# Kernel optimization log

Hardware: AMD Instinct MI355X
Metric: run time of the kernel (lower is better)

Reference implementation:

```python
import jax, jax.numpy as jnp
import numpy as np

B, N_MM, N_V, N_A = 2, 256, 64, 128
DIM, HEADS, ATTN_RATIO, MLP_RATIO = 1024, 16, 0.25, 4.0
INNER = int(DIM * ATTN_RATIO)          # 256
HID = int(DIM * MLP_RATIO)             # 4096
SCALE = (DIM // HEADS) ** -0.5         # faithful to source: uses dim//num_heads
EPS = 1e-5


def setup_inputs() -> dict:
    key = jax.random.key(0)
    ks = jax.random.split(key, 16)
    s = 0.02
    return {
        "xmm": jax.random.normal(ks[0], (B, N_MM, DIM), jnp.float32),
        "xv": jax.random.normal(ks[1], (B, N_V, DIM), jnp.float32),
        "xa": jax.random.normal(ks[2], (B, N_A, DIM), jnp.float32),
        "ln_mm_w": jnp.ones((DIM,), jnp.float32),
        "ln_mm_b": jnp.zeros((DIM,), jnp.float32),
        "ln_v_w": jnp.ones((DIM,), jnp.float32),
        "ln_v_b": jnp.zeros((DIM,), jnp.float32),
        "ln_a_w": jnp.ones((DIM,), jnp.float32),
        "ln_a_b": jnp.zeros((DIM,), jnp.float32),
        "Wq": jax.random.normal(ks[3], (DIM, INNER), jnp.float32) * s,
        "Wkv": jax.random.normal(ks[4], (2 * DIM, 2 * INNER), jnp.float32) * s,
        "Wproj": jax.random.normal(ks[5], (INNER, DIM), jnp.float32) * s,
        "bproj": jnp.zeros((DIM,), jnp.float32),
        "ln_mlp_w": jnp.ones((DIM,), jnp.float32),
        "ln_mlp_b": jnp.zeros((DIM,), jnp.float32),
        "W1": jax.random.normal(ks[6], (DIM, HID), jnp.float32) * s,
        "b1": jnp.zeros((HID,), jnp.float32),
        "W2": jax.random.normal(ks[7], (HID, DIM), jnp.float32) * s,
        "b2": jnp.zeros((DIM,), jnp.float32),
    }


def _ln(x, w, b):
    m = x.mean(-1, keepdims=True)
    v = ((x - m) ** 2).mean(-1, keepdims=True)
    return (x - m) / jnp.sqrt(v + EPS) * w + b


def reference(xmm, xv, xa, ln_mm_w, ln_mm_b, ln_v_w, ln_v_b, ln_a_w, ln_a_b,
              Wq, Wkv, Wproj, bproj, ln_mlp_w, ln_mlp_b, W1, b1, W2, b2):
    hd = INNER // HEADS
    src_mm = _ln(xmm, ln_mm_w, ln_mm_b)
    src_v = _ln(xv, ln_v_w, ln_v_b)
    src_a = _ln(xa, ln_a_w, ln_a_b)

    # kv(x_va) where x_va = cat([xv broadcast over N_a, xa broadcast over N_v], -1).
    # Equivalent to projecting each stream separately and broadcast-adding:
    kv_v = src_v @ Wkv[:DIM]            # [B, N_v, 2*INNER]
    kv_a = src_a @ Wkv[DIM:]            # [B, N_a, 2*INNER]
    kv = kv_v[:, :, None, :] + kv_a[:, None, :, :]          # [B, N_v, N_a, 2*INNER]
    kv = kv.reshape(B, N_V * N_A, 2, HEADS, hd)
    k = kv[:, :, 0].transpose(0, 2, 1, 3)                   # [B, H, N_va, hd]
    v = kv[:, :, 1].transpose(0, 2, 1, 3)

    q = (src_mm @ Wq).reshape(B, N_MM, HEADS, hd).transpose(0, 2, 1, 3)

    attn = jnp.einsum('bhqd,bhkd->bhqk', q, k) * SCALE
    attn = jax.nn.softmax(attn, axis=-1)
    out = jnp.einsum('bhqk,bhkd->bhqd', attn, v)
    out = out.transpose(0, 2, 1, 3).reshape(B, N_MM, INNER)
    out = out @ Wproj + bproj

    xmm = xmm + out
    h = _ln(xmm, ln_mlp_w, ln_mlp_b)
    h = jax.nn.gelu(h @ W1 + b1, approximate=False) @ W2 + b2
    return xmm + h
```

## Files before the change

### kernel.cpp

```cpp
#include <hip/hip_runtime.h>
#include <hip/hip_bf16.h>
#include <math.h>


typedef unsigned short ushort_t;
typedef __attribute__((ext_vector_type(8))) __bf16 bf16x8;
typedef __attribute__((ext_vector_type(4))) float f32x4;

#define DEVFN static __device__ __forceinline__

DEVFN ushort_t f2bf(float f) {
    unsigned int x = __float_as_uint(f);
    unsigned int r = x + 0x7FFFu + ((x >> 16) & 1u);
    return (ushort_t)(r >> 16);
}
DEVFN void unpack8(uint4 dv, float* dst) {
    unsigned int ws[4] = {dv.x, dv.y, dv.z, dv.w};
#pragma unroll
    for (int i = 0; i < 4; i++) {
        dst[2 * i] = __uint_as_float(ws[i] << 16);
        dst[2 * i + 1] = __uint_as_float(ws[i] & 0xFFFF0000u);
    }
}

DEVFN void ln_body(const float* __restrict__ x, const float* __restrict__ w,
                   const float* __restrict__ b, ushort_t* __restrict__ out,
                   int row) {
    const float4* xr4 = (const float4*)(x + (size_t)row * 1024);
    ushort_t* orow = out + (size_t)row * 1024;
    int tid = threadIdx.x;
    float4 v4 = xr4[tid];
    float s = v4.x + v4.y + v4.z + v4.w;
    float ss = v4.x * v4.x + v4.y * v4.y + v4.z * v4.z + v4.w * v4.w;
#pragma unroll
    for (int off = 32; off > 0; off >>= 1) {
        s += __shfl_down(s, off);
        ss += __shfl_down(ss, off);
    }
    __shared__ float red[8];
    if ((tid & 63) == 0) {
        red[tid >> 6] = s;
        red[4 + (tid >> 6)] = ss;
    }
    __syncthreads();
    s = red[0] + red[1] + red[2] + red[3];
    ss = red[4] + red[5] + red[6] + red[7];
    float mean = s * (1.f / 1024.f);
    float var = ss * (1.f / 1024.f) - mean * mean;
    float rstd = rsqrtf(var + 1e-5f);
    const float4 w4 = ((const float4*)w)[tid];
    const float4 b4 = ((const float4*)b)[tid];
    union { ushort_t u[4]; uint2 v; } pk;
    pk.u[0] = f2bf((v4.x - mean) * rstd * w4.x + b4.x);
    pk.u[1] = f2bf((v4.y - mean) * rstd * w4.y + b4.y);
    pk.u[2] = f2bf((v4.z - mean) * rstd * w4.z + b4.z);
    pk.u[3] = f2bf((v4.w - mean) * rstd * w4.w + b4.w);
    *(uint2*)(&orow[tid * 4]) = pk.v;
}

__global__ __launch_bounds__(256) void ln_kernel(
    const float* __restrict__ x, const float* __restrict__ w,
    const float* __restrict__ b, ushort_t* __restrict__ out) {
    ln_body(x, w, b, out, blockIdx.x);
}

struct LNSeg {
    const float* x; const float* w; const float* b; ushort_t* out; int start;
};
struct TDesc { const float* in; ushort_t* out; int R, C, nx, start; };

DEVFN void transpose_body(TDesc d, int t, ushort_t* lds) {
    int bx = (t % d.nx) * 64;
    int by = (t / d.nx) * 64;
    int tid = threadIdx.x;
#pragma unroll
    for (int it = 0; it < 4; it++) {
        int idx = it * 256 + tid;
        int r = idx >> 4;
        int c4 = (idx & 15) << 2;
        float4 v = *(const float4*)(&d.in[(size_t)(by + r) * d.C + bx + c4]);
        float vals[4] = {v.x, v.y, v.z, v.w};
#pragma unroll
        for (int j = 0; j < 4; j++) {
            int c = c4 + j;
            int rs = (r + (((c >> 2) & 7) << 3)) & 63;
            lds[c * 64 + rs] = f2bf(vals[j]);
        }
    }
    __syncthreads();
#pragma unroll
    for (int it = 0; it < 2; it++) {
        int idx = it * 256 + tid;
        int c = idx >> 3;
        int l8 = idx & 7;
        int rs = ((l8 << 3) + (((c >> 2) & 7) << 3)) & 63;
        uint4 val = *(const uint4*)(&lds[c * 64 + rs]);
        *(uint4*)(&d.out[(size_t)(bx + c) * d.R + by + (l8 << 3)]) = val;
    }
    __syncthreads();
}

__global__ __launch_bounds__(256) void prep_kernel(LNSeg l0, LNSeg l1,
                                                   LNSeg l2, TDesc d0,
                                                   TDesc d1) {
    int id = blockIdx.x;
    if (id < 896) {
        LNSeg s = (id >= l2.start) ? l2 : ((id >= l1.start) ? l1 : l0);
        ln_body(s.x, s.w, s.b, s.out, id - s.start);
        return;
    }
    id -= 896;
    __shared__ ushort_t tile[64 * 64];
    TDesc d = (id >= d1.start) ? d1 : d0;
    transpose_body(d, id - d.start, tile);
}

template <int EPI, typename OutT>
DEVFN void gemm64_core(const ushort_t* __restrict__ A, int lda,
                       const ushort_t* __restrict__ B, int ldb,
                       OutT* __restrict__ C, int ldc,
                       const float* __restrict__ bias,
                       const float* __restrict__ resid, int K, int m0, int n0,
                       ushort_t* As, ushort_t* Bs) {
    constexpr int LS = 72;
    int tid = threadIdx.x;
    int wave = tid >> 6, lane = tid & 63;
    int wm = wave >> 1, wn = wave & 1;
    int quad = lane >> 4, l16 = lane & 15;

    f32x4 acc[2][2];
#pragma unroll
    for (int i = 0; i < 2; i++)
#pragma unroll
        for (int j = 0; j < 2; j++) acc[i][j] = (f32x4){0.f, 0.f, 0.f, 0.f};

    int r = tid >> 3;
    int c = tid & 7;
    const ushort_t* Ap = A + (size_t)(m0 + r) * lda + c * 8;
    const ushort_t* Bp = B + (size_t)(n0 + r) * ldb + c * 8;
    const ushort_t* Ap2 = Ap + (size_t)32 * lda;
    const ushort_t* Bp2 = Bp + (size_t)32 * ldb;
    uint4 ra = *(const uint4*)Ap, ra2 = *(const uint4*)Ap2;
    uint4 rb = *(const uint4*)Bp, rb2 = *(const uint4*)Bp2;

    for (int k0 = 0; k0 < K; k0 += 64) {
        *(uint4*)(&As[r * LS + c * 8]) = ra;
        *(uint4*)(&As[(r + 32) * LS + c * 8]) = ra2;
        *(uint4*)(&Bs[r * LS + c * 8]) = rb;
        *(uint4*)(&Bs[(r + 32) * LS + c * 8]) = rb2;
        __syncthreads();
        if (k0 + 64 < K) {
            ra = *(const uint4*)(Ap + k0 + 64);
            ra2 = *(const uint4*)(Ap2 + k0 + 64);
            rb = *(const uint4*)(Bp + k0 + 64);
            rb2 = *(const uint4*)(Bp2 + k0 + 64);
        }
#pragma unroll
        for (int ks = 0; ks < 2; ks++) {
            bf16x8 af[2], bfr[2];
#pragma unroll
            for (int i = 0; i < 2; i++)
                af[i] = *(const bf16x8*)(
                    &As[(wm * 32 + i * 16 + l16) * LS + ks * 32 + quad * 8]);
#pragma unroll
            for (int j = 0; j < 2; j++)
                bfr[j] = *(const bf16x8*)(
                    &Bs[(wn * 32 + j * 16 + l16) * LS + ks * 32 + quad * 8]);
#pragma unroll
            for (int i = 0; i < 2; i++)
#pragma unroll
                for (int j = 0; j < 2; j++)
                    acc[i][j] = __builtin_amdgcn_mfma_f32_16x16x32_bf16(
                        af[i], bfr[j], acc[i][j], 0, 0, 0);
        }
        __syncthreads();
    }

#pragma unroll
    for (int i = 0; i < 2; i++)
#pragma unroll
        for (int j = 0; j < 2; j++) {
            int col = n0 + wn * 32 + j * 16 + l16;
            int rbase = m0 + wm * 32 + i * 16 + quad * 4;
            float bv = (EPI == 2 || EPI == 3) ? bias[col] : 0.f;
#pragma unroll
            for (int rr = 0; rr < 4; rr++) {
                int row = rbase + rr;
                float vv = acc[i][j][rr] + bv;
                if (EPI == 2) vv = 0.5f * vv * (1.f + erff(vv * 0.70710678118654752f));
                if (EPI == 3) vv += resid[(size_t)row * ldc + col];
                if constexpr (sizeof(OutT) == 2)
                    C[(size_t)row * ldc + col] = (OutT)f2bf(vv);
                else
                    C[(size_t)row * ldc + col] = vv;
            }
        }
}

template <int EPI, typename OutT>
__global__ __launch_bounds__(256) void gemm64(
    const ushort_t* __restrict__ A, int lda, const ushort_t* __restrict__ Bt,
    int ldb, OutT* __restrict__ C, int ldc, const float* __restrict__ bias,
    const float* __restrict__ resid, int Kper, int sliceStride) {
    __shared__ ushort_t As[64 * 72];
    __shared__ ushort_t Bs[64 * 72];
    int z = blockIdx.z;
    gemm64_core<EPI, OutT>(A + (size_t)z * Kper, lda, Bt + (size_t)z * Kper,
                           ldb, C + (size_t)z * sliceStride, ldc, bias, resid,
                           Kper, blockIdx.y * 64, blockIdx.x * 64, As, Bs);
}

struct GSeg {
    const ushort_t* A; const ushort_t* B; ushort_t* C;
    int lda, ldb, ldc, nx, start;
};

__global__ __launch_bounds__(256) void projT_kernel(GSeg s0, GSeg s1, GSeg s2,
                                                    TDesc d0, TDesc d1,
                                                    TDesc d2, int K) {
    __shared__ ushort_t As[64 * 72];
    __shared__ ushort_t Bs[64 * 72];
    int id = blockIdx.x;
    if (id < 80) {
        GSeg s = (id >= s2.start) ? s2 : ((id >= s1.start) ? s1 : s0);
        int t = id - s.start;
        int n0 = (t % s.nx) * 64;
        int m0 = (t / s.nx) * 64;
        gemm64_core<0, ushort_t>(s.A, s.lda, s.B, s.ldb, s.C, s.ldc, nullptr,
                                 nullptr, K, m0, n0, As, Bs);
        return;
    }
    id -= 80;
    TDesc d = (id >= d2.start) ? d2 : ((id >= d1.start) ? d1 : d0);
    transpose_body(d, id - d.start, As);
}

__global__ __launch_bounds__(256) void reduce_mlp2(
    const float* __restrict__ P, const float* __restrict__ y,
    const float* __restrict__ b2, float* __restrict__ out) {
    int i = blockIdx.x * 256 + threadIdx.x;
    const float4* p = (const float4*)P;
    float4 a = p[i], b = p[i + 131072], cc = p[i + 2 * 131072],
           d = p[i + 3 * 131072];
    float4 yy = ((const float4*)y)[i];
    float4 bb = ((const float4*)b2)[i & 255];
    float4 o;
    o.x = a.x + b.x + cc.x + d.x + yy.x + bb.x;
    o.y = a.y + b.y + cc.y + d.y + yy.y + bb.y;
    o.z = a.z + b.z + cc.z + d.z + yy.z + bb.z;
    o.w = a.w + b.w + cc.w + d.w + yy.w + bb.w;
    ((float4*)out)[i] = o;
}

__global__ __launch_bounds__(256) void attn_kernel(
    const ushort_t* __restrict__ q, const ushort_t* __restrict__ kvv,
    const ushort_t* __restrict__ kva, ushort_t* __restrict__ out) {
    int bh = blockIdx.x;
    int b = bh >> 4, h = bh & 15;
    int tid = threadIdx.x;

    __shared__ float Kv[64][16], Vv[64][16], Ka[128][16], Va[128][16];

    {
        int row = tid >> 2, seg = (tid >> 1) & 1, half = tid & 1;
        const ushort_t* src =
            kvv + (size_t)(b * 64 + row) * 512 + seg * 256 + h * 16 + half * 8;
        float* dst = (seg ? Vv[row] : Kv[row]) + half * 8;
        unpack8(*(const uint4*)src, dst);
    }
#pragma unroll
    for (int t2 = 0; t2 < 2; t2++) {
        int t = tid + t2 * 256;
        int row = t >> 2, seg = (t >> 1) & 1, half = t & 1;
        const ushort_t* src =
            kva + (size_t)(b * 128 + row) * 512 + seg * 256 + h * 16 + half * 8;
        float* dst = (seg ? Va[row] : Ka[row]) + half * 8;
        unpack8(*(const uint4*)src, dst);
    }
    __syncthreads();

    int qlocal = tid >> 2;
    int dg = tid & 3;
    int qrow = blockIdx.y * 64 + qlocal;
    const ushort_t* qp = q + (size_t)(b * 256 + qrow) * 256 + h * 16 + dg * 4;
    uint2 qu = *(const uint2*)qp;
    float4 qv;
    qv.x = __uint_as_float(qu.x << 16) * 0.125f;
    qv.y = __uint_as_float(qu.x & 0xFFFF0000u) * 0.125f;
    qv.z = __uint_as_float(qu.y << 16) * 0.125f;
    qv.w = __uint_as_float(qu.y & 0xFFFF0000u) * 0.125f;

    const float4* Kv4 = (const float4*)Kv;
    const float4* Vv4 = (const float4*)Vv;
    const float4* Ka4 = (const float4*)Ka;
    const float4* Va4 = (const float4*)Va;

    float4 ov = {0.f, 0.f, 0.f, 0.f};
    float den = 0.f;
#pragma unroll 8
    for (int i = 0; i < 64; i++) {
        float4 kk = Kv4[i * 4 + dg];
        float part = qv.x * kk.x + qv.y * kk.y + qv.z * kk.z + qv.w * kk.w;
        part += __shfl_xor(part, 1);
        part += __shfl_xor(part, 2);
        float p = __expf(part);
        den += p;
        float4 vv = Vv4[i * 4 + dg];
        ov.x += p * vv.x; ov.y += p * vv.y; ov.z += p * vv.z; ov.w += p * vv.w;
    }
    float4 oa = {0.f, 0.f, 0.f, 0.f};
    float dena = 0.f;
#pragma unroll 8
    for (int i = 0; i < 128; i++) {
        float4 kk = Ka4[i * 4 + dg];
        float part = qv.x * kk.x + qv.y * kk.y + qv.z * kk.z + qv.w * kk.w;
        part += __shfl_xor(part, 1);
        part += __shfl_xor(part, 2);
        float p = __expf(part);
        dena += p;
        float4 vv = Va4[i * 4 + dg];
        oa.x += p * vv.x; oa.y += p * vv.y; oa.z += p * vv.z; oa.w += p * vv.w;
    }

    float rv = 1.f / den, ra = 1.f / dena;
    union { ushort_t u[4]; uint2 v; } pk;
    pk.u[0] = f2bf(ov.x * rv + oa.x * ra);
    pk.u[1] = f2bf(ov.y * rv + oa.y * ra);
    pk.u[2] = f2bf(ov.z * rv + oa.z * ra);
    pk.u[3] = f2bf(ov.w * rv + oa.w * ra);
    *(uint2*)(out + (size_t)(b * 256 + qrow) * 256 + h * 16 + dg * 4) = pk.v;
}

extern "C" void kernel_launch(void* const* d_in, const int* in_sizes, int n_in,
                              void* d_out, int out_size, void* d_ws,
                              size_t ws_size, hipStream_t stream) {
    const float* xmm = (const float*)d_in[0];
    const float* xv = (const float*)d_in[1];
    const float* xa = (const float*)d_in[2];
    const float* ln_mm_w = (const float*)d_in[3];
    const float* ln_mm_b = (const float*)d_in[4];
    const float* ln_v_w = (const float*)d_in[5];
    const float* ln_v_b = (const float*)d_in[6];
    const float* ln_a_w = (const float*)d_in[7];
    const float* ln_a_b = (const float*)d_in[8];
    const float* Wq = (const float*)d_in[9];
    const float* Wkv = (const float*)d_in[10];
    const float* Wproj = (const float*)d_in[11];
    const float* bproj = (const float*)d_in[12];
    const float* ln_mlp_w = (const float*)d_in[13];
    const float* ln_mlp_b = (const float*)d_in[14];
    const float* W1 = (const float*)d_in[15];
    const float* b1 = (const float*)d_in[16];
    const float* W2 = (const float*)d_in[17];
    const float* b2 = (const float*)d_in[18];
    float* outp = (float*)d_out;

    char* w = (char*)d_ws;
    ushort_t* xmmN = (ushort_t*)w;    w += 512 * 1024 * 2;
    ushort_t* xvN = (ushort_t*)w;     w += 128 * 1024 * 2;
    ushort_t* xaN = (ushort_t*)w;     w += 256 * 1024 * 2;
    ushort_t* Wqt = (ushort_t*)w;     w += 256 * 1024 * 2;
    ushort_t* Wkvt = (ushort_t*)w;    w += 512 * 2048 * 2;
    ushort_t* Wprojt = (ushort_t*)w;  w += 1024 * 256 * 2;
    ushort_t* W1t = (ushort_t*)w;     w += 4096 * 1024 * 2;
    ushort_t* W2t = (ushort_t*)w;     w += 1024 * 4096 * 2;
    ushort_t* qout = (ushort_t*)w;    w += 512 * 256 * 2;
    ushort_t* kvvb = (ushort_t*)w;    w += 128 * 512 * 2;
    ushort_t* kvab = (ushort_t*)w;    w += 256 * 512 * 2;
    ushort_t* attnout = (ushort_t*)w; w += 512 * 256 * 2;
    float* y = (float*)w;             w += 512 * 1024 * 4;
    ushort_t* h0 = (ushort_t*)w;      w += 512 * 1024 * 2;
    ushort_t* g = (ushort_t*)w;       w += 512 * 4096 * 2;
    float* P = (float*)w;             w += 4 * 512 * 1024 * 4;

    LNSeg L0{xmm, ln_mm_w, ln_mm_b, xmmN, 0};
    LNSeg L1{xv, ln_v_w, ln_v_b, xvN, 512};
    LNSeg L2{xa, ln_a_w, ln_a_b, xaN, 640};
    TDesc TQ{Wq, Wqt, 1024, 256, 4, 0};
    TDesc TKV{Wkv, Wkvt, 2048, 512, 8, 64};
    prep_kernel<<<896 + 320, 256, 0, stream>>>(L0, L1, L2, TQ, TKV);

    GSeg G0{xmmN, Wqt, qout, 1024, 1024, 256, 4, 0};
    GSeg G1{xvN, Wkvt, kvvb, 1024, 2048, 512, 8, 32};
    GSeg G2{xaN, Wkvt + 1024, kvab, 1024, 2048, 512, 8, 48};
    TDesc TP{Wproj, Wprojt, 256, 1024, 16, 0};
    TDesc T1{W1, W1t, 1024, 4096, 64, 64};
    TDesc T2{W2, W2t, 4096, 1024, 16, 1088};
    projT_kernel<<<80 + 2112, 256, 0, stream>>>(G0, G1, G2, TP, T1, T2, 1024);

    attn_kernel<<<dim3(32, 4), 256, 0, stream>>>(qout, kvvb, kvab, attnout);

    gemm64<3, float><<<dim3(16, 8, 1), 256, 0, stream>>>(
        attnout, 256, Wprojt, 256, y, 1024, bproj, xmm, 256, 0);

    ln_kernel<<<512, 256, 0, stream>>>(y, ln_mlp_w, ln_mlp_b, h0);

    gemm64<2, ushort_t><<<dim3(64, 8, 1), 256, 0, stream>>>(
        h0, 1024, W1t, 1024, g, 4096, b1, nullptr, 1024, 0);

    gemm64<4, float><<<dim3(16, 8, 4), 256, 0, stream>>>(
        g, 4096, W2t, 4096, P, 1024, nullptr, nullptr, 1024, 512 * 1024);

    reduce_mlp2<<<512, 256, 0, stream>>>(P, y, b2, outp);

    (void)in_sizes; (void)n_in; (void)out_size; (void)ws_size;
}
```

Before: 184.2 us.

## Fuse attention, projection, LN and MLP stages into one persistent kernel with grid barriers

Six separate tail launches (attention, output projection, MLP LayerNorm, two MLP GEMMs, split-K reduction) are merged into one 512-block kernel. Stages are separated by software grid-wide barriers built on atomic counters in workspace, which are zeroed by a memset each call. The aim is to remove per-launch overhead and the idle gaps between small kernels. The cost is spin-wait barriers: they assume all 512 blocks are resident at once (launch bounds request 2 blocks per CU), and the loop breaks out after a fixed retry count, which could silently break correctness if co-residency fails.

```diff
diff --git a/kernel.cpp b/kernel.cpp
--- a/kernel.cpp
+++ b/kernel.cpp
@@ -21,6 +21,22 @@
         dst[2 * i] = __uint_as_float(ws[i] << 16);
         dst[2 * i + 1] = __uint_as_float(ws[i] & 0xFFFF0000u);
     }
+}
+
+DEVFN void gsync(unsigned int* c) {
+    __syncthreads();
+    if (threadIdx.x == 0) {
+        __threadfence();
+        __hip_atomic_fetch_add(c, 1u, __ATOMIC_RELEASE, __HIP_MEMORY_SCOPE_AGENT);
+        unsigned int nb = gridDim.x;
+        unsigned int tries = 0;
+        while (__hip_atomic_load(c, __ATOMIC_ACQUIRE, __HIP_MEMORY_SCOPE_AGENT) < nb) {
+            __builtin_amdgcn_s_sleep(1);
+            if (++tries > (1u << 22)) break;
+        }
+        __threadfence();
+    }
+    __syncthreads();
 }
 
 DEVFN void ln_body(const float* __restrict__ x, const float* __restrict__ w,
@@ -58,12 +74,6 @@
     *(uint2*)(&orow[tid * 4]) = pk.v;
 }
 
-__global__ __launch_bounds__(256) void ln_kernel(
-    const float* __restrict__ x, const float* __restrict__ w,
-    const float* __restrict__ b, ushort_t* __restrict__ out) {
-    ln_body(x, w, b, out, blockIdx.x);
-}
-
 struct LNSeg {
     const float* x; const float* w; const float* b; ushort_t* out; int start;
 };
@@ -195,19 +205,6 @@
                     C[(size_t)row * ldc + col] = vv;
             }
         }
-}
-
-template <int EPI, typename OutT>
-__global__ __launch_bounds__(256) void gemm64(
-    const ushort_t* __restrict__ A, int lda, const ushort_t* __restrict__ Bt,
-    int ldb, OutT* __restrict__ C, int ldc, const float* __restrict__ bias,
-    const float* __restrict__ resid, int Kper, int sliceStride) {
-    __shared__ ushort_t As[64 * 72];
-    __shared__ ushort_t Bs[64 * 72];
-    int z = blockIdx.z;
-    gemm64_core<EPI, OutT>(A + (size_t)z * Kper, lda, Bt + (size_t)z * Kper,
-                           ldb, C + (size_t)z * sliceStride, ldc, bias, resid,
-                           Kper, blockIdx.y * 64, blockIdx.x * 64, As, Bs);
 }
 
 struct GSeg {
@@ -235,31 +232,16 @@
     transpose_body(d, id - d.start, As);
 }
 
-__global__ __launch_bounds__(256) void reduce_mlp2(
-    const float* __restrict__ P, const float* __restrict__ y,
-    const float* __restrict__ b2, float* __restrict__ out) {
-    int i = blockIdx.x * 256 + threadIdx.x;
-    const float4* p = (const float4*)P;
-    float4 a = p[i], b = p[i + 131072], cc = p[i + 2 * 131072],
-           d = p[i + 3 * 131072];
-    float4 yy = ((const float4*)y)[i];
-    float4 bb = ((const float4*)b2)[i & 255];
-    float4 o;
-    o.x = a.x + b.x + cc.x + d.x + yy.x + bb.x;
-    o.y = a.y + b.y + cc.y + d.y + yy.y + bb.y;
-    o.z = a.z + b.z + cc.z + d.z + yy.z + bb.z;
-    o.w = a.w + b.w + cc.w + d.w + yy.w + bb.w;
-    ((float4*)out)[i] = o;
-}
-
-__global__ __launch_bounds__(256) void attn_kernel(
-    const ushort_t* __restrict__ q, const ushort_t* __restrict__ kvv,
-    const ushort_t* __restrict__ kva, ushort_t* __restrict__ out) {
-    int bh = blockIdx.x;
+DEVFN void attn_body(const ushort_t* __restrict__ q,
+                     const ushort_t* __restrict__ kvv,
+                     const ushort_t* __restrict__ kva,
+                     ushort_t* __restrict__ out, int bh, int qc, float* sm) {
     int b = bh >> 4, h = bh & 15;
     int tid = threadIdx.x;
-
-    __shared__ float Kv[64][16], Vv[64][16], Ka[128][16], Va[128][16];
+    float (*Kv)[16] = (float(*)[16])sm;
+    float (*Vv)[16] = (float(*)[16])(sm + 64 * 16);
+    float (*Ka)[16] = (float(*)[16])(sm + 2 * 64 * 16);
+    float (*Va)[16] = (float(*)[16])(sm + 2 * 64 * 16 + 128 * 16);
 
     {
         int row = tid >> 2, seg = (tid >> 1) & 1, half = tid & 1;
@@ -281,7 +263,7 @@
 
     int qlocal = tid >> 2;
     int dg = tid & 3;
-    int qrow = blockIdx.y * 64 + qlocal;
+    int qrow = qc * 64 + qlocal;
     const ushort_t* qp = q + (size_t)(b * 256 + qrow) * 256 + h * 16 + dg * 4;
     uint2 qu = *(const uint2*)qp;
     float4 qv;
@@ -329,6 +311,74 @@
     pk.u[2] = f2bf(ov.z * rv + oa.z * ra);
     pk.u[3] = f2bf(ov.w * rv + oa.w * ra);
     *(uint2*)(out + (size_t)(b * 256 + qrow) * 256 + h * 16 + dg * 4) = pk.v;
+}
+
+DEVFN void reduce_body(const float* __restrict__ P, const float* __restrict__ y,
+                       const float* __restrict__ b2, float* __restrict__ out,
+                       int blk) {
+    int i = blk * 256 + threadIdx.x;
+    const float4* p = (const float4*)P;
+    float4 a = p[i], b = p[i + 131072], cc = p[i + 2 * 131072],
+           d = p[i + 3 * 131072];
+    float4 yy = ((const float4*)y)[i];
+    float4 bb = ((const float4*)b2)[i & 255];
+    float4 o;
+    o.x = a.x + b.x + cc.x + d.x + yy.x + bb.x;
+    o.y = a.y + b.y + cc.y + d.y + yy.y + bb.y;
+    o.z = a.z + b.z + cc.z + d.z + yy.z + bb.z;
+    o.w = a.w + b.w + cc.w + d.w + yy.w + bb.w;
+    ((float4*)out)[i] = o;
+}
+
+struct TailArgs {
+    const ushort_t* qout; const ushort_t* kvvb; const ushort_t* kvab;
+    ushort_t* attnout;
+    const ushort_t* Wprojt; const float* bproj; const float* xmm; float* y;
+    const float* ln_mlp_w; const float* ln_mlp_b; ushort_t* h0;
+    const ushort_t* W1t; const float* b1; ushort_t* g;
+    const ushort_t* W2t; float* P;
+    const float* b2; float* outp;
+    unsigned int* bars;
+};
+
+__global__ __launch_bounds__(256, 2) void tail_kernel(TailArgs a) {
+    __shared__ __align__(16) char smem[24576];
+    ushort_t* As = (ushort_t*)smem;
+    ushort_t* Bs = (ushort_t*)(smem + 9216);
+    int bid = blockIdx.x;
+
+    if (bid < 128) attn_body(a.qout, a.kvvb, a.kvab, a.attnout, bid & 31,
+                             bid >> 5, (float*)smem);
+    gsync(&a.bars[0]);
+
+    if (bid < 128) {
+        int n0 = (bid % 16) * 64, m0 = (bid / 16) * 64;
+        gemm64_core<3, float>(a.attnout, 256, a.Wprojt, 256, a.y, 1024,
+                              a.bproj, a.xmm, 256, m0, n0, As, Bs);
+    }
+    gsync(&a.bars[1]);
+
+    ln_body(a.y, a.ln_mlp_w, a.ln_mlp_b, a.h0, bid);
+    gsync(&a.bars[2]);
+
+    {
+        int n0 = (bid % 64) * 64, m0 = (bid / 64) * 64;
+        gemm64_core<2, ushort_t>(a.h0, 1024, a.W1t, 1024, a.g, 4096, a.b1,
+                                 nullptr, 1024, m0, n0, As, Bs);
+    }
+    gsync(&a.bars[3]);
+
+    {
+        int z = bid >> 7, rr = bid & 127;
+        int n0 = (rr % 16) * 64, m0 = (rr / 16) * 64;
+        gemm64_core<4, float>(a.g + (size_t)z * 1024, 4096,
+                              a.W2t + (size_t)z * 1024, 4096,
+                              a.P + (size_t)z * 512 * 1024, 1024, nullptr,
+                              nullptr, 1024, m0, n0, As, Bs);
+    }
+    gsync(&a.bars[4]);
+
+    reduce_body(a.P, a.y, a.b2, a.outp, bid);
 }
 
 extern "C" void kernel_launch(void* const* d_in, const int* in_sizes, int n_in,
@@ -356,6 +406,7 @@
     float* outp = (float*)d_out;
 
     char* w = (char*)d_ws;
+    unsigned int* bars = (unsigned int*)w; w += 256;
     ushort_t* xmmN = (ushort_t*)w;    w += 512 * 1024 * 2;
     ushort_t* xvN = (ushort_t*)w;     w += 128 * 1024 * 2;
     ushort_t* xaN = (ushort_t*)w;     w += 256 * 1024 * 2;
@@ -373,6 +424,8 @@
     ushort_t* g = (ushort_t*)w;       w += 512 * 4096 * 2;
     float* P = (float*)w;             w += 4 * 512 * 1024 * 4;
 
+    hipMemsetAsync(bars, 0, 64, stream);
+
     LNSeg L0{xmm, ln_mm_w, ln_mm_b, xmmN, 0};
     LNSeg L1{xv, ln_v_w, ln_v_b, xvN, 512};
     LNSeg L2{xa, ln_a_w, ln_a_b, xaN, 640};
@@ -388,20 +441,13 @@
     TDesc T2{W2, W2t, 4096, 1024, 16, 1088};
     projT_kernel<<<80 + 2112, 256, 0, stream>>>(G0, G1, G2, TP, T1, T2, 1024);
 
-    attn_kernel<<<dim3(32, 4), 256, 0, stream>>>(qout, kvvb, kvab, attnout);
-
-    gemm64<3, float><<<dim3(16, 8, 1), 256, 0, stream>>>(
-        attnout, 256, Wprojt, 256, y, 1024, bproj, xmm, 256, 0);
-
-    ln_kernel<<<512, 256, 0, stream>>>(y, ln_mlp_w, ln_mlp_b, h0);
-
-    gemm64<2, ushort_t><<<dim3(64, 8, 1), 256, 0, stream>>>(
-        h0, 1024, W1t, 1024, g, 4096, b1, nullptr, 1024, 0);
-
-    gemm64<4, float><<<dim3(16, 8, 4), 256, 0, stream>>>(
-        g, 4096, W2t, 4096, P, 1024, nullptr, nullptr, 1024, 512 * 1024);
-
-    reduce_mlp2<<<512, 256, 0, stream>>>(P, y, b2, outp);
+    TailArgs TA{qout, kvvb, kvab, attnout,
+                Wprojt, bproj, xmm, y,
+                ln_mlp_w, ln_mlp_b, h0,
+                W1t, b1, g,
+                W2t, P,
+                b2, outp, bars};
+    tail_kernel<<<512, 256, 0, stream>>>(TA);
 
     (void)in_sizes; (void)n_in; (void)out_size; (void)ws_size;
 }
```

After: 512.4 us. 2.78x slower.

## Fuse MLP LayerNorm into GEMMs and split-K reduction into last block

Applied to the files above, without the earlier changes.

The proj GEMM epilogue now writes per-tile row sum and sum-of-squares partials. The W1 GEMM reads those partials to normalize y on the fly, which removes the separate LayerNorm kernel and the h0 buffer. The split-K reduction for W2 is folded into the GEMM through an atomic counter: the last of the four slices per tile does the sum, which removes another launch. The costs are a variance computed as E[x²]-mean² from partials, an fp32 A-operand load with per-element conversion inside the W1 GEMM loop, and counter resets placed in the attention kernel.

```diff
diff --git a/kernel.cpp b/kernel.cpp
--- a/kernel.cpp
+++ b/kernel.cpp
@@ -58,12 +58,6 @@
     *(uint2*)(&orow[tid * 4]) = pk.v;
 }
 
-__global__ __launch_bounds__(256) void ln_kernel(
-    const float* __restrict__ x, const float* __restrict__ w,
-    const float* __restrict__ b, ushort_t* __restrict__ out) {
-    ln_body(x, w, b, out, blockIdx.x);
-}
-
 struct LNSeg {
     const float* x; const float* w; const float* b; ushort_t* out; int start;
 };
@@ -121,7 +115,8 @@
                        OutT* __restrict__ C, int ldc,
                        const float* __restrict__ bias,
                        const float* __restrict__ resid, int K, int m0, int n0,
-                       ushort_t* As, ushort_t* Bs) {
+                       ushort_t* As, ushort_t* Bs,
+                       float* __restrict__ stats = nullptr) {
     constexpr int LS = 72;
     int tid = threadIdx.x;
     int wave = tid >> 6, lane = tid & 63;
@@ -176,38 +171,58 @@
         __syncthreads();
     }
 
+    float srow[2][4] = {{0.f, 0.f, 0.f, 0.f}, {0.f, 0.f, 0.f, 0.f}};
+    float ssrow[2][4] = {{0.f, 0.f, 0.f, 0.f}, {0.f, 0.f, 0.f, 0.f}};
+
 #pragma unroll
     for (int i = 0; i < 2; i++)
 #pragma unroll
         for (int j = 0; j < 2; j++) {
             int col = n0 + wn * 32 + j * 16 + l16;
             int rbase = m0 + wm * 32 + i * 16 + quad * 4;
-            float bv = (EPI == 2 || EPI == 3) ? bias[col] : 0.f;
+            float bv = (EPI == 5) ? bias[col] : 0.f;
 #pragma unroll
             for (int rr = 0; rr < 4; rr++) {
                 int row = rbase + rr;
                 float vv = acc[i][j][rr] + bv;
-                if (EPI == 2) vv = 0.5f * vv * (1.f + erff(vv * 0.70710678118654752f));
-                if (EPI == 3) vv += resid[(size_t)row * ldc + col];
+                if constexpr (EPI == 5) {
+                    vv += resid[(size_t)row * ldc + col];
+                    srow[i][rr] += vv;
+                    ssrow[i][rr] += vv * vv;
+                }
                 if constexpr (sizeof(OutT) == 2)
                     C[(size_t)row * ldc + col] = (OutT)f2bf(vv);
                 else
                     C[(size_t)row * ldc + col] = vv;
             }
         }
-}
-
-template <int EPI, typename OutT>
-__global__ __launch_bounds__(256) void gemm64(
-    const ushort_t* __restrict__ A, int lda, const ushort_t* __restrict__ Bt,
-    int ldb, OutT* __restrict__ C, int ldc, const float* __restrict__ bias,
-    const float* __restrict__ resid, int Kper, int sliceStride) {
-    __shared__ ushort_t As[64 * 72];
-    __shared__ ushort_t Bs[64 * 72];
-    int z = blockIdx.z;
-    gemm64_core<EPI, OutT>(A + (size_t)z * Kper, lda, Bt + (size_t)z * Kper,
-                           ldb, C + (size_t)z * sliceStride, ldc, bias, resid,
-                           Kper, blockIdx.y * 64, blockIdx.x * 64, As, Bs);
+
+    if constexpr (EPI == 5) {
+        float* ls = (float*)As;
+#pragma unroll
+        for (int i = 0; i < 2; i++)
+#pragma unroll
+            for (int rr = 0; rr < 4; rr++) {
+                float s = srow[i][rr], ss = ssrow[i][rr];
+#pragma unroll
+                for (int m = 1; m < 16; m <<= 1) {
+                    s += __shfl_xor(s, m);
+                    ss += __shfl_xor(ss, m);
+                }
+                if (l16 == 0) {
+                    int rl = wm * 32 + i * 16 + quad * 4 + rr;
+                    ls[rl * 4 + wn * 2 + 0] = s;
+                    ls[rl * 4 + wn * 2 + 1] = ss;
+                }
+            }
+        __syncthreads();
+        if (tid < 64) {
+            float s = ls[tid * 4 + 0] + ls[tid * 4 + 2];
+            float ss = ls[tid * 4 + 1] + ls[tid * 4 + 3];
+            stats[(size_t)(m0 + tid) * 2 + 0] = s;
+            stats[(size_t)(m0 + tid) * 2 + 1] = ss;
+        }
+    }
 }
 
 struct GSeg {
@@ -235,26 +250,173 @@
     transpose_body(d, id - d.start, As);
 }
 
-__global__ __launch_bounds__(256) void reduce_mlp2(
-    const float* __restrict__ P, const float* __restrict__ y,
-    const float* __restrict__ b2, float* __restrict__ out) {
-    int i = blockIdx.x * 256 + threadIdx.x;
-    const float4* p = (const float4*)P;
-    float4 a = p[i], b = p[i + 131072], cc = p[i + 2 * 131072],
-           d = p[i + 3 * 131072];
-    float4 yy = ((const float4*)y)[i];
-    float4 bb = ((const float4*)b2)[i & 255];
-    float4 o;
-    o.x = a.x + b.x + cc.x + d.x + yy.x + bb.x;
-    o.y = a.y + b.y + cc.y + d.y + yy.y + bb.y;
-    o.z = a.z + b.z + cc.z + d.z + yy.z + bb.z;
-    o.w = a.w + b.w + cc.w + d.w + yy.w + bb.w;
-    ((float4*)out)[i] = o;
+__global__ __launch_bounds__(256) void ygemm_kernel(
+    const ushort_t* __restrict__ A, const ushort_t* __restrict__ Bt,
+    float* __restrict__ y, const float* __restrict__ bproj,
+    const float* __restrict__ xmm, float* __restrict__ pstats) {
+    __shared__ ushort_t As[64 * 72];
+    __shared__ ushort_t Bs[64 * 72];
+    gemm64_core<5, float>(A, 256, Bt, 256, y, 1024, bproj, xmm, 256,
+                          blockIdx.y * 64, blockIdx.x * 64, As, Bs,
+                          pstats + (size_t)blockIdx.x * 512 * 2);
+}
+
+__global__ __launch_bounds__(256) void mlp1_kernel(
+    const float* __restrict__ y, const float* __restrict__ pstats,
+    const float* __restrict__ lnw, const float* __restrict__ lnb,
+    const ushort_t* __restrict__ W1t, const float* __restrict__ b1,
+    ushort_t* __restrict__ g) {
+    constexpr int LS = 40;
+    __shared__ ushort_t As[64 * LS];
+    __shared__ ushort_t Bs[64 * LS];
+    __shared__ float wls[1024], bls[1024];
+    int tid = threadIdx.x;
+    int m0 = blockIdx.y * 64, n0 = blockIdx.x * 64;
+
+    ((float4*)wls)[tid] = ((const float4*)lnw)[tid];
+    ((float4*)bls)[tid] = ((const float4*)lnb)[tid];
+
+    int r = tid >> 2, c = tid & 3;
+    float s = 0.f, ss = 0.f;
+#pragma unroll
+    for (int k = 0; k < 4; k++) {
+        size_t o = ((size_t)(c * 4 + k) * 512 + (m0 + r)) * 2;
+        s += pstats[o];
+        ss += pstats[o + 1];
+    }
+    s += __shfl_xor(s, 1); ss += __shfl_xor(ss, 1);
+    s += __shfl_xor(s, 2); ss += __shfl_xor(ss, 2);
+    float mr = s * (1.f / 1024.f);
+    float var = ss * (1.f / 1024.f) - mr * mr;
+    float rs = rsqrtf(var + 1e-5f);
+
+    int wave = tid >> 6, lane = tid & 63;
+    int wm = wave >> 1, wn = wave & 1;
+    int quad = lane >> 4, l16 = lane & 15;
+
+    f32x4 acc[2][2];
+#pragma unroll
+    for (int i = 0; i < 2; i++)
+#pragma unroll
+        for (int j = 0; j < 2; j++) acc[i][j] = (f32x4){0.f, 0.f, 0.f, 0.f};
+
+    const float* Ay = y + (size_t)(m0 + r) * 1024 + c * 8;
+    const ushort_t* Bp = W1t + (size_t)(n0 + r) * 1024 + c * 8;
+    float4 ya0 = *(const float4*)Ay;
+    float4 ya1 = *(const float4*)(Ay + 4);
+    uint4 rb = *(const uint4*)Bp;
+    __syncthreads();
+
+    for (int k0 = 0; k0 < 1024; k0 += 32) {
+        float4 w0 = *(const float4*)&wls[k0 + c * 8];
+        float4 w1 = *(const float4*)&wls[k0 + c * 8 + 4];
+        float4 bb0 = *(const float4*)&bls[k0 + c * 8];
+        float4 bb1 = *(const float4*)&bls[k0 + c * 8 + 4];
+        union { ushort_t u[8]; uint4 v; } pa;
+        pa.u[0] = f2bf((ya0.x - mr) * rs * w0.x + bb0.x);
+        pa.u[1] = f2bf((ya0.y - mr) * rs * w0.y + bb0.y);
+        pa.u[2] = f2bf((ya0.z - mr) * rs * w0.z + bb0.z);
+        pa.u[3] = f2bf((ya0.w - mr) * rs * w0.w + bb0.w);
+        pa.u[4] = f2bf((ya1.x - mr) * rs * w1.x + bb1.x);
+        pa.u[5] = f2bf((ya1.y - mr) * rs * w1.y + bb1.y);
+        pa.u[6] = f2bf((ya1.z - mr) * rs * w1.z + bb1.z);
+        pa.u[7] = f2bf((ya1.w - mr) * rs * w1.w + bb1.w);
+        *(uint4*)(&As[r * LS + c * 8]) = pa.v;
+        *(uint4*)(&Bs[r * LS + c * 8]) = rb;
+        __syncthreads();
+        if (k0 + 32 < 1024) {
+            ya0 = *(const float4*)(Ay + k0 + 32);
+            ya1 = *(const float4*)(Ay + k0 + 36);
+            rb = *(const uint4*)(Bp + k0 + 32);
+        }
+        bf16x8 af[2], bfr[2];
+#pragma unroll
+        for (int i = 0; i < 2; i++)
+            af[i] = *(const bf16x8*)(&As[(wm * 32 + i * 16 + l16) * LS + quad * 8]);
+#pragma unroll
+        for (int j = 0; j < 2; j++)
+            bfr[j] = *(const bf16x8*)(&Bs[(wn * 32 + j * 16 + l16) * LS + quad * 8]);
+#pragma unroll
+        for (int i = 0; i < 2; i++)
+#pragma unroll
+            for (int j = 0; j < 2; j++)
+                acc[i][j] = __builtin_amdgcn_mfma_f32_16x16x32_bf16(
+                    af[i], bfr[j], acc[i][j], 0, 0, 0);
+        __syncthreads();
+    }
+
+#pragma unroll
+    for (int i = 0; i < 2; i++)
+#pragma unroll
+        for (int j = 0; j < 2; j++) {
+            int col = n0 + wn * 32 + j * 16 + l16;
+            int rbase = m0 + wm * 32 + i * 16 + quad * 4;
+            float bv = b1[col];
+#pragma unroll
+            for (int rr = 0; rr < 4; rr++) {
+                int row = rbase + rr;
+                float vv = acc[i][j][rr] + bv;
+                vv = 0.5f * vv * (1.f + erff(vv * 0.70710678118654752f));
+                g[(size_t)row * 4096 + col] = f2bf(vv);
+            }
+        }
+}
+
+__global__ __launch_bounds__(256) void mlp2_kernel(
+    const ushort_t* __restrict__ g, const ushort_t* __restrict__ W2t,
+    float* __restrict__ P, const float* __restrict__ y,
+    const float* __restrict__ b2, float* __restrict__ out,
+    unsigned int* __restrict__ cnt) {
+    __shared__ ushort_t As[64 * 72];
+    __shared__ ushort_t Bs[64 * 72];
+    int z = blockIdx.z;
+    int m0 = blockIdx.y * 64, n0 = blockIdx.x * 64;
+    gemm64_core<4, float>(g + (size_t)z * 1024, 4096, W2t + (size_t)z * 1024,
+                          4096, P + (size_t)z * 512 * 1024, 1024, nullptr,
+                          nullptr, 1024, m0, n0, As, Bs);
+
+    __shared__ int lastf;
+    __syncthreads();
+    if (threadIdx.x == 0) {
+        __threadfence();
+        unsigned int old = __hip_atomic_fetch_add(
+            &cnt[blockIdx.y * 16 + blockIdx.x], 1u, __ATOMIC_ACQ_REL,
+            __HIP_MEMORY_SCOPE_AGENT);
+        lastf = (old == 3u);
+        if (lastf) __threadfence();
+    }
+    __syncthreads();
+    if (!lastf) return;
+
+    int tid = threadIdx.x;
+#pragma unroll
+    for (int k = 0; k < 4; k++) {
+        int idx4 = tid * 4 + k;
+        int row = m0 + (idx4 >> 4);
+        int c0 = n0 + (idx4 & 15) * 4;
+        size_t off = (size_t)row * 1024 + c0;
+        float4 a = *(const float4*)(P + off);
+        float4 b = *(const float4*)(P + 524288 + off);
+        float4 cc = *(const float4*)(P + 1048576 + off);
+        float4 d = *(const float4*)(P + 1572864 + off);
+        float4 yy = *(const float4*)(y + off);
+        float4 bb = *(const float4*)(b2 + c0);
+        float4 o;
+        o.x = a.x + b.x + cc.x + d.x + yy.x + bb.x;
+        o.y = a.y + b.y + cc.y + d.y + yy.y + bb.y;
+        o.z = a.z + b.z + cc.z + d.z + yy.z + bb.z;
+        o.w = a.w + b.w + cc.w + d.w + yy.w + bb.w;
+        *(float4*)(out + off) = o;
+    }
 }
 
 __global__ __launch_bounds__(256) void attn_kernel(
     const ushort_t* __restrict__ q, const ushort_t* __restrict__ kvv,
-    const ushort_t* __restrict__ kva, ushort_t* __restrict__ out) {
+    const ushort_t* __restrict__ kva, ushort_t* __restrict__ out,
+    unsigned int* __restrict__ cnt) {
+    if (blockIdx.x == 0 && blockIdx.y == 0 && threadIdx.x < 128)
+        cnt[threadIdx.x] = 0u;
+
     int bh = blockIdx.x;
     int b = bh >> 4, h = bh & 15;
     int tid = threadIdx.x;
@@ -356,6 +518,8 @@
     float* outp = (float*)d_out;
 
     char* w = (char*)d_ws;
+    unsigned int* cnt = (unsigned int*)w; w += 1024;
+    float* pstats = (float*)w;        w += 16 * 512 * 2 * 4;
     ushort_t* xmmN = (ushort_t*)w;    w += 512 * 1024 * 2;
     ushort_t* xvN = (ushort_t*)w;     w += 128 * 1024 * 2;
     ushort_t* xaN = (ushort_t*)w;     w += 256 * 1024 * 2;
@@ -369,7 +533,6 @@
     ushort_t* kvab = (ushort_t*)w;    w += 256 * 512 * 2;
     ushort_t* attnout = (ushort_t*)w; w += 512 * 256 * 2;
     float* y = (float*)w;             w += 512 * 1024 * 4;
-    ushort_t* h0 = (ushort_t*)w;      w += 512 * 1024 * 2;
     ushort_t* g = (ushort_t*)w;       w += 512 * 4096 * 2;
     float* P = (float*)w;             w += 4 * 512 * 1024 * 4;
 
@@ -388,20 +551,17 @@
     TDesc T2{W2, W2t, 4096, 1024, 16, 1088};
     projT_kernel<<<80 + 2112, 256, 0, stream>>>(G0, G1, G2, TP, T1, T2, 1024);
 
-    attn_kernel<<<dim3(32, 4), 256, 0, stream>>>(qout, kvvb, kvab, attnout);
-
-    gemm64<3, float><<<dim3(16, 8, 1), 256, 0, stream>>>(
-        attnout, 256, Wprojt, 256, y, 1024, bproj, xmm, 256, 0);
-
-    ln_kernel<<<512, 256, 0, stream>>>(y, ln_mlp_w, ln_mlp_b, h0);
-
-    gemm64<2, ushort_t><<<dim3(64, 8, 1), 256, 0, stream>>>(
-        h0, 1024, W1t, 1024, g, 4096, b1, nullptr, 1024, 0);
-
-    gemm64<4, float><<<dim3(16, 8, 4), 256, 0, stream>>>(
-        g, 4096, W2t, 4096, P, 1024, nullptr, nullptr, 1024, 512 * 1024);
-
-    reduce_mlp2<<<512, 256, 0, stream>>>(P, y, b2, outp);
+    attn_kernel<<<dim3(32, 4), 256, 0, stream>>>(qout, kvvb, kvab, attnout,
+                                                 cnt);
+
+    ygemm_kernel<<<dim3(16, 8), 256, 0, stream>>>(attnout, Wprojt, y, bproj,
+                                                  xmm, pstats);
+
+    mlp1_kernel<<<dim3(64, 8), 256, 0, stream>>>(y, pstats, ln_mlp_w,
+                                                 ln_mlp_b, W1t, b1, g);
+
+    mlp2_kernel<<<dim3(16, 8, 4), 256, 0, stream>>>(g, W2t, P, y, b2, outp,
+                                                    cnt);
 
     (void)in_sizes; (void)n_in; (void)out_size; (void)ws_size;
 }
```

Measured after the change: 224.0 us. 1.22x slower.

## Double-buffer GEMM LDS tiles and spread weight transposes across later kernels

Applied to the files above, without the earlier changes.

The GEMM core now alternates between two LDS buffers, which removes the second barrier in each K iteration. The W1 and W2 transposes no longer run inside the projection kernel. The W1 transpose is fused with the attention kernel and the W2 transpose with the MLP1 GEMM, so the transposes overlap compute that would otherwise underfill the GPU. The cost is double the shared memory per GEMM block, which may lower occupancy. The attention and MLP1 blocks also now share launches with many transpose blocks.

```diff
diff --git a/kernel.cpp b/kernel.cpp
--- a/kernel.cpp
+++ b/kernel.cpp
@@ -123,6 +123,7 @@
                        const float* __restrict__ resid, int K, int m0, int n0,
                        ushort_t* As, ushort_t* Bs) {
     constexpr int LS = 72;
+    constexpr int BUF = 64 * LS;
     int tid = threadIdx.x;
     int wave = tid >> 6, lane = tid & 63;
     int wm = wave >> 1, wn = wave & 1;
@@ -143,11 +144,14 @@
     uint4 ra = *(const uint4*)Ap, ra2 = *(const uint4*)Ap2;
     uint4 rb = *(const uint4*)Bp, rb2 = *(const uint4*)Bp2;
 
+    int p = 0;
     for (int k0 = 0; k0 < K; k0 += 64) {
-        *(uint4*)(&As[r * LS + c * 8]) = ra;
-        *(uint4*)(&As[(r + 32) * LS + c * 8]) = ra2;
-        *(uint4*)(&Bs[r * LS + c * 8]) = rb;
-        *(uint4*)(&Bs[(r + 32) * LS + c * 8]) = rb2;
+        ushort_t* Ab = As + p * BUF;
+        ushort_t* Bb = Bs + p * BUF;
+        *(uint4*)(&Ab[r * LS + c * 8]) = ra;
+        *(uint4*)(&Ab[(r + 32) * LS + c * 8]) = ra2;
+        *(uint4*)(&Bb[r * LS + c * 8]) = rb;
+        *(uint4*)(&Bb[(r + 32) * LS + c * 8]) = rb2;
         __syncthreads();
         if (k0 + 64 < K) {
             ra = *(const uint4*)(Ap + k0 + 64);
@@ -161,11 +165,11 @@
 #pragma unroll
             for (int i = 0; i < 2; i++)
                 af[i] = *(const bf16x8*)(
-                    &As[(wm * 32 + i * 16 + l16) * LS + ks * 32 + quad * 8]);
+                    &Ab[(wm * 32 + i * 16 + l16) * LS + ks * 32 + quad * 8]);
 #pragma unroll
             for (int j = 0; j < 2; j++)
                 bfr[j] = *(const bf16x8*)(
-                    &Bs[(wn * 32 + j * 16 + l16) * LS + ks * 32 + quad * 8]);
+                    &Bb[(wn * 32 + j * 16 + l16) * LS + ks * 32 + quad * 8]);
 #pragma unroll
             for (int i = 0; i < 2; i++)
 #pragma unroll
@@ -173,7 +177,7 @@
                     acc[i][j] = __builtin_amdgcn_mfma_f32_16x16x32_bf16(
                         af[i], bfr[j], acc[i][j], 0, 0, 0);
         }
-        __syncthreads();
+        p ^= 1;
     }
 
 #pragma unroll
@@ -202,8 +206,8 @@
     const ushort_t* __restrict__ A, int lda, const ushort_t* __restrict__ Bt,
     int ldb, OutT* __restrict__ C, int ldc, const float* __restrict__ bias,
     const float* __restrict__ resid, int Kper, int sliceStride) {
-    __shared__ ushort_t As[64 * 72];
-    __shared__ ushort_t Bs[64 * 72];
+    __shared__ ushort_t As[2 * 64 * 72];
+    __shared__ ushort_t Bs[2 * 64 * 72];
     int z = blockIdx.z;
     gemm64_core<EPI, OutT>(A + (size_t)z * Kper, lda, Bt + (size_t)z * Kper,
                            ldb, C + (size_t)z * sliceStride, ldc, bias, resid,
@@ -216,10 +220,9 @@
 };
 
 __global__ __launch_bounds__(256) void projT_kernel(GSeg s0, GSeg s1, GSeg s2,
-                                                    TDesc d0, TDesc d1,
-                                                    TDesc d2, int K) {
-    __shared__ ushort_t As[64 * 72];
-    __shared__ ushort_t Bs[64 * 72];
+                                                    TDesc dP, int K) {
+    __shared__ ushort_t As[2 * 64 * 72];
+    __shared__ ushort_t Bs[2 * 64 * 72];
     int id = blockIdx.x;
     if (id < 80) {
         GSeg s = (id >= s2.start) ? s2 : ((id >= s1.start) ? s1 : s0);
@@ -230,9 +233,115 @@
                                  nullptr, K, m0, n0, As, Bs);
         return;
     }
-    id -= 80;
-    TDesc d = (id >= d2.start) ? d2 : ((id >= d1.start) ? d1 : d0);
-    transpose_body(d, id - d.start, As);
+    transpose_body(dP, id - 80, As);
+}
+
+DEVFN void attn_body(const ushort_t* __restrict__ q,
+                     const ushort_t* __restrict__ kvv,
+                     const ushort_t* __restrict__ kva,
+                     ushort_t* __restrict__ out, int bh, int qc, float* sm) {
+    int b = bh >> 4, h = bh & 15;
+    int tid = threadIdx.x;
+    float (*Kv)[16] = (float(*)[16])sm;
+    float (*Vv)[16] = (float(*)[16])(sm + 64 * 16);
+    float (*Ka)[16] = (float(*)[16])(sm + 2 * 64 * 16);
+    float (*Va)[16] = (float(*)[16])(sm + 2 * 64 * 16 + 128 * 16);
+
+    {
+        int row = tid >> 2, seg = (tid >> 1) & 1, half = tid & 1;
+        const ushort_t* src =
+            kvv + (size_t)(b * 64 + row) * 512 + seg * 256 + h * 16 + half * 8;
+        float* dst = (seg ? Vv[row] : Kv[row]) + half * 8;
+        unpack8(*(const uint4*)src, dst);
+    }
+#pragma unroll
+    for (int t2 = 0; t2 < 2; t2++) {
+        int t = tid + t2 * 256;
+        int row = t >> 2, seg = (t >> 1) & 1, half = t & 1;
+        const ushort_t* src =
+            kva + (size_t)(b * 128 + row) * 512 + seg * 256 + h * 16 + half * 8;
+        float* dst = (seg ? Va[row] : Ka[row]) + half * 8;
+        unpack8(*(const uint4*)src, dst);
+    }
+    __syncthreads();
+
+    int qlocal = tid >> 2;
+    int dg = tid & 3;
+    int qrow = qc * 64 + qlocal;
+    const ushort_t* qp = q + (size_t)(b * 256 + qrow) * 256 + h * 16 + dg * 4;
+    uint2 qu = *(const uint2*)qp;
+    float4 qv;
+    qv.x = __uint_as_float(qu.x << 16) * 0.125f;
+    qv.y = __uint_as_float(qu.x & 0xFFFF0000u) * 0.125f;
+    qv.z = __uint_as_float(qu.y << 16) * 0.125f;
+    qv.w = __uint_as_float(qu.y & 0xFFFF0000u) * 0.125f;
+
+    const float4* Kv4 = (const float4*)Kv;
+    const float4* Vv4 = (const float4*)Vv;
+    const float4* Ka4 = (const float4*)Ka;
+    const float4* Va4 = (const float4*)Va;
+
+    float4 ov = {0.f, 0.f, 0.f, 0.f};
+    float den = 0.f;
+#pragma unroll 8
+    for (int i = 0; i < 64; i++) {
+        float4 kk = Kv4[i * 4 + dg];
+        float part = qv.x * kk.x + qv.y * kk.y + qv.z * kk.z + qv.w * kk.w;
+        part += __shfl_xor(part, 1);
+        part += __shfl_xor(part, 2);
+        float p = __expf(part);
+        den += p;
+        float4 vv = Vv4[i * 4 + dg];
+        ov.x += p * vv.x; ov.y += p * vv.y; ov.z += p * vv.z; ov.w += p * vv.w;
+    }
+    float4 oa = {0.f, 0.f, 0.f, 0.f};
+    float dena = 0.f;
+#pragma unroll 8
+    for (int i = 0; i < 128; i++) {
+        float4 kk = Ka4[i * 4 + dg];
+        float part = qv.x * kk.x + qv.y * kk.y + qv.z * kk.z + qv.w * kk.w;
+        part += __shfl_xor(part, 1);
+        part += __shfl_xor(part, 2);
+        float p = __expf(part);
+        dena += p;
+        float4 vv = Va4[i * 4 + dg];
+        oa.x += p * vv.x; oa.y += p * vv.y; oa.z += p * vv.z; oa.w += p * vv.w;
+    }
+
+    float rv = 1.f / den, ra = 1.f / dena;
+    union { ushort_t u[4]; uint2 v; } pk;
+    pk.u[0] = f2bf(ov.x * rv + oa.x * ra);
+    pk.u[1] = f2bf(ov.y * rv + oa.y * ra);
+    pk.u[2] = f2bf(ov.z * rv + oa.z * ra);
+    pk.u[3] = f2bf(ov.w * rv + oa.w * ra);
+    *(uint2*)(out + (size_t)(b * 256 + qrow) * 256 + h * 16 + dg * 4) = pk.v;
+}
+
+__global__ __launch_bounds__(256) void attnT_kernel(
+    const ushort_t* __restrict__ q, const ushort_t* __restrict__ kvv,
+    const ushort_t* __restrict__ kva, ushort_t* __restrict__ out, TDesc d1) {
+    __shared__ __align__(16) char smem[24576];
+    int id = blockIdx.x;
+    if (id < 128) {
+        attn_body(q, kvv, kva, out, id & 31, id >> 5, (float*)smem);
+        return;
+    }
+    transpose_body(d1, id - 128, (ushort_t*)smem);
+}
+
+__global__ __launch_bounds__(256) void mlp1T_kernel(
+    const ushort_t* __restrict__ h0, const ushort_t* __restrict__ W1t,
+    const float* __restrict__ b1, ushort_t* __restrict__ g, TDesc d2) {
+    __shared__ ushort_t As[2 * 64 * 72];
+    __shared__ ushort_t Bs[2 * 64 * 72];
+    int id = blockIdx.x;
+    if (id < 512) {
+        int n0 = (id % 64) * 64, m0 = (id / 64) * 64;
+        gemm64_core<2, ushort_t>(h0, 1024, W1t, 1024, g, 4096, b1, nullptr,
+                                 1024, m0, n0, As, Bs);
+        return;
+    }
+    transpose_body(d2, id - 512, As);
 }
 
 __global__ __launch_bounds__(256) void reduce_mlp2(
@@ -250,85 +359,6 @@
     o.z = a.z + b.z + cc.z + d.z + yy.z + bb.z;
     o.w = a.w + b.w + cc.w + d.w + yy.w + bb.w;
     ((float4*)out)[i] = o;
-}
-
-__global__ __launch_bounds__(256) void attn_kernel(
-    const ushort_t* __restrict__ q, const ushort_t* __restrict__ kvv,
-    const ushort_t* __restrict__ kva, ushort_t* __restrict__ out) {
-    int bh = blockIdx.x;
-    int b = bh >> 4, h = bh & 15;
-    int tid = threadIdx.x;
-
-    __shared__ float Kv[64][16], Vv[64][16], Ka[128][16], Va[128][16];
-
-    {
-        int row = tid >> 2, seg = (tid >> 1) & 1, half = tid & 1;
-        const ushort_t* src =
-            kvv + (size_t)(b * 64 + row) * 512 + seg * 256 + h * 16 + half * 8;
-        float* dst = (seg ? Vv[row] : Kv[row]) + half * 8;
-        unpack8(*(const uint4*)src, dst);
-    }
-#pragma unroll
-    for (int t2 = 0; t2 < 2; t2++) {
-        int t = tid + t2 * 256;
-        int row = t >> 2, seg = (t >> 1) & 1, half = t & 1;
-        const ushort_t* src =
-            kva + (size_t)(b * 128 + row) * 512 + seg * 256 + h * 16 + half * 8;
-        float* dst = (seg ? Va[row] : Ka[row]) + half * 8;
-        unpack8(*(const uint4*)src, dst);
-    }
-    __syncthreads();
-
-    int qlocal = tid >> 2;
-    int dg = tid & 3;
-    int qrow = blockIdx.y * 64 + qlocal;
-    const ushort_t* qp = q + (size_t)(b * 256 + qrow) * 256 + h * 16 + dg * 4;
-    uint2 qu = *(const uint2*)qp;
-    float4 qv;
-    qv.x = __uint_as_float(qu.x << 16) * 0.125f;
-    qv.y = __uint_as_float(qu.x & 0xFFFF0000u) * 0.125f;
-    qv.z = __uint_as_float(qu.y << 16) * 0.125f;
-    qv.w = __uint_as_float(qu.y & 0xFFFF0000u) * 0.125f;
-
-    const float4* Kv4 = (const float4*)Kv;
-    const float4* Vv4 = (const float4*)Vv;
-    const float4* Ka4 = (const float4*)Ka;
-    const float4* Va4 = (const float4*)Va;
-
-    float4 ov = {0.f, 0.f, 0.f, 0.f};
-    float den = 0.f;
-#pragma unroll 8
-    for (int i = 0; i < 64; i++) {
-        float4 kk = Kv4[i * 4 + dg];
-        float part = qv.x * kk.x + qv.y * kk.y + qv.z * kk.z + qv.w * kk.w;
-        part += __shfl_xor(part, 1);
-        part += __shfl_xor(part, 2);
-        float p = __expf(part);
-        den += p;
-        float4 vv = Vv4[i * 4 + dg];
-        ov.x += p * vv.x; ov.y += p * vv.y; ov.z += p * vv.z; ov.w += p * vv.w;
-    }
-    float4 oa = {0.f, 0.f, 0.f, 0.f};
-    float dena = 0.f;
-#pragma unroll 8
-    for (int i = 0; i < 128; i++) {
-        float4 kk = Ka4[i * 4 + dg];
-        float part = qv.x * kk.x + qv.y * kk.y + qv.z * kk.z + qv.w * kk.w;
-        part += __shfl_xor(part, 1);
-        part += __shfl_xor(part, 2);
-        float p = __expf(part);
-        dena += p;
-        float4 vv = Va4[i * 4 + dg];
-        oa.x += p * vv.x; oa.y += p * vv.y; oa.z += p * vv.z; oa.w += p * vv.w;
-    }
-
-    float rv = 1.f / den, ra = 1.f / dena;
-    union { ushort_t u[4]; uint2 v; } pk;
-    pk.u[0] = f2bf(ov.x * rv + oa.x * ra);
-    pk.u[1] = f2bf(ov.y * rv + oa.y * ra);
-    pk.u[2] = f2bf(ov.z * rv + oa.z * ra);
-    pk.u[3] = f2bf(ov.w * rv + oa.w * ra);
-    *(uint2*)(out + (size_t)(b * 256 + qrow) * 256 + h * 16 + dg * 4) = pk.v;
 }
 
 extern "C" void kernel_launch(void* const* d_in, const int* in_sizes, int n_in,
@@ -384,19 +414,19 @@
     GSeg G1{xvN, Wkvt, kvvb, 1024, 2048, 512, 8, 32};
     GSeg G2{xaN, Wkvt + 1024, kvab, 1024, 2048, 512, 8, 48};
     TDesc TP{Wproj, Wprojt, 256, 1024, 16, 0};
-    TDesc T1{W1, W1t, 1024, 4096, 64, 64};
-    TDesc T2{W2, W2t, 4096, 1024, 16, 1088};
-    projT_kernel<<<80 + 2112, 256, 0, stream>>>(G0, G1, G2, TP, T1, T2, 1024);
-
-    attn_kernel<<<dim3(32, 4), 256, 0, stream>>>(qout, kvvb, kvab, attnout);
+    projT_kernel<<<80 + 64, 256, 0, stream>>>(G0, G1, G2, TP, 1024);
+
+    TDesc T1{W1, W1t, 1024, 4096, 64, 0};
+    attnT_kernel<<<128 + 1024, 256, 0, stream>>>(qout, kvvb, kvab, attnout,
+                                                 T1);
 
     gemm64<3, float><<<dim3(16, 8, 1), 256, 0, stream>>>(
         attnout, 256, Wprojt, 256, y, 1024, bproj, xmm, 256, 0);
 
     ln_kernel<<<512, 256, 0, stream>>>(y, ln_mlp_w, ln_mlp_b, h0);
 
-    gemm64<2, ushort_t><<<dim3(64, 8, 1), 256, 0, stream>>>(
-        h0, 1024, W1t, 1024, g, 4096, b1, nullptr, 1024, 0);
+    TDesc T2{W2, W2t, 4096, 1024, 16, 0};
+    mlp1T_kernel<<<512 + 1024, 256, 0, stream>>>(h0, W1t, b1, g, T2);
 
     gemm64<4, float><<<dim3(16, 8, 4), 256, 0, stream>>>(
         g, 4096, W2t, 4096, P, 1024, nullptr, nullptr, 1024, 512 * 1024);
```

Measured after the change: 182.9 us. About the same (-0.7%).
